# Kernel optimization log

Measured on AMD Instinct MI355X. Metric: run time of the kernel, lower is better.

Reference implementation:

```python
import jax, jax.numpy as jnp
import numpy as np


def make_coord(h, w):
    # LIIF cell-center coordinates in (-1, 1), first axis = rows (height)
    y = -1.0 + (2.0 * jnp.arange(h, dtype=jnp.float32) + 1.0) / h
    x = -1.0 + (2.0 * jnp.arange(w, dtype=jnp.float32) + 1.0) / w
    yy, xx = jnp.meshgrid(y, x, indexing='ij')
    return jnp.stack([yy, xx], axis=-1)  # (h, w, 2)


def gather_nearest(img, coord):
    """Nearest grid_sample, align_corners=False, padding_mode='zeros'.
    img: (b, c, h, w); coord: (b, n, 2) with [...,0]->height, [...,1]->width.
    Returns (b, n, c)."""
    b, c, h, w = img.shape
    iy = jnp.round(((coord[..., 0] + 1.0) * h - 1.0) / 2.0)
    ix = jnp.round(((coord[..., 1] + 1.0) * w - 1.0) / 2.0)
    valid = (iy >= 0) & (iy < h) & (ix >= 0) & (ix < w)
    iyc = jnp.clip(iy, 0, h - 1).astype(jnp.int32)
    ixc = jnp.clip(ix, 0, w - 1).astype(jnp.int32)
    idx = iyc * w + ixc                                  # (b, n)
    flat = img.reshape(b, c, h * w)
    out = jnp.take_along_axis(flat, idx[:, None, :], axis=2)  # (b, c, n)
    out = jnp.transpose(out, (0, 2, 1))                  # (b, n, c)
    return jnp.where(valid[..., None], out, 0.0)


def mlp(x, w1, b1, w2, b2, w3, b3):
    x = jax.nn.relu(x @ w1 + b1)
    x = jax.nn.relu(x @ w2 + b2)
    return x @ w3 + b3


def query_freq(feat, coord, guide, params):
    b, c, h, w = feat.shape
    H, W = guide.shape[2], guide.shape[3]
    feat_coord = make_coord(h, w)                        # (h, w, 2)
    fc_img = jnp.broadcast_to(jnp.transpose(feat_coord, (2, 0, 1))[None], (b, 2, h, w))
    q_guide = gather_nearest(guide, coord)               # (b, N, guide_dim)
    scale = jnp.array([h, w], dtype=feat.dtype)
    preds = []
    for vx in (-1.0, 1.0):
        for vy in (-1.0, 1.0):
            off = jnp.array([vx / h, vy / w], dtype=feat.dtype)
            c_ = coord + off
            q_feat = gather_nearest(feat, c_)            # (b, N, feat_dim)
            q_coord = gather_nearest(fc_img, c_)         # (b, N, 2)
            rel = (coord - q_coord) * scale              # (b, N, 2)
            inp = jnp.concatenate([q_feat, q_guide, rel], axis=-1)
            preds.append(mlp(inp, *params))              # (b, N, NIR_dim)
    preds = jnp.stack(preds, axis=-1)                    # (b, N, NIR_dim, 4)
    weight = jax.nn.softmax(preds[:, :, -1, :], axis=-1) # (b, N, 4)
    ret = jnp.sum(preds[:, :, :-1, :] * weight[:, :, None, :], axis=-1)  # (b, N, NIR_dim-1)
    return jnp.transpose(ret, (0, 2, 1)).reshape(b, -1, H, W)


def setup_inputs() -> dict:
    key = jax.random.key(0)
    ks = jax.random.split(key, 16)
    b, fd, gd = 8, 128, 128
    h = w = 64
    H = W = 128
    feat = jax.random.normal(ks[0], (b, fd, h, w), dtype=jnp.float32)
    hr_guide = jax.random.normal(ks[1], (b, gd, H, W), dtype=jnp.float32)
    coord = jnp.broadcast_to(make_coord(H, W).reshape(1, H * W, 2), (b, H * W, 2))
    in_dim, h1, h2, out_dim = fd + gd + 2, 256, 128, 33

    def lin(k, i, o):
        return jax.random.normal(k, (i, o), dtype=jnp.float32) / np.sqrt(i).astype(np.float32)

    d = {"feat": feat, "coord": coord, "hr_guide": hr_guide,
         "a_w1": lin(ks[2], in_dim, h1), "a_b1": jnp.zeros((h1,), jnp.float32),
         "a_w2": lin(ks[3], h1, h2),     "a_b2": jnp.zeros((h2,), jnp.float32),
         "a_w3": lin(ks[4], h2, out_dim),"a_b3": jnp.zeros((out_dim,), jnp.float32),
         "p_w1": lin(ks[5], in_dim, h1), "p_b1": jnp.zeros((h1,), jnp.float32),
         "p_w2": lin(ks[6], h1, h2),     "p_b2": jnp.zeros((h2,), jnp.float32),
         "p_w3": lin(ks[7], h2, out_dim),"p_b3": jnp.zeros((out_dim,), jnp.float32)}
    return d


def reference(feat, coord, hr_guide, a_w1, a_b1, a_w2, a_b2, a_w3, a_b3,
              p_w1, p_b1, p_w2, p_b2, p_w3, p_b3):
    feat_f = jnp.fft.fftn(feat, axes=(-2, -1))
    guide_f = jnp.fft.fftn(hr_guide, axes=(-2, -1))
    feat_mag, feat_pha = jnp.abs(feat_f), jnp.angle(feat_f)
    guide_mag, guide_pha = jnp.abs(guide_f), jnp.angle(guide_f)
    mag = query_freq(feat_mag, coord, guide_mag, (a_w1, a_b1, a_w2, a_b2, a_w3, a_b3))
    pha = query_freq(feat_pha, coord, guide_pha, (p_w1, p_b1, p_w2, p_b2, p_w3, p_b3))
    ffted = jax.lax.complex(mag * jnp.cos(pha), mag * jnp.sin(pha))
    return jnp.abs(jnp.fft.ifftn(ffted, axes=(-2, -1)))
```

## Files before the change

kernel.cpp:

```cpp
#include <hip/hip_runtime.h>
#include <cmath>

#define TPB 256

static constexpr int   Bn   = 8;
static constexpr int   FD   = 128, GD = 128;
static constexpr int   FH   = 64,  FW = 64;
static constexpr int   GH   = 128, GW = 128;
static constexpr int   NPIX = GH * GW;
static constexpr long  ROWS = (long)Bn * NPIX;
static constexpr int   NH1  = 256, NH2 = 128, NOUT = 33;
static constexpr float TWO_PI = 6.28318530717958647692f;

typedef __attribute__((ext_vector_type(8))) __bf16 bf16x8;
typedef __attribute__((ext_vector_type(4))) float  f32x4;

__global__ __launch_bounds__(TPB)
void k_meta(const float* __restrict__ coord, int* __restrict__ idxb,
            float2* __restrict__ relb) {
    int t = blockIdx.x * TPB + threadIdx.x;
    if (t >= NPIX * 4) return;
    int pix = t >> 2, o = t & 3;
    float cy = coord[pix * 2 + 0], cx = coord[pix * 2 + 1];
    float vx = (o < 2) ? -1.f : 1.f;
    float vy = (o & 1) ? 1.f : -1.f;
    float cyo = cy + vx / 64.f, cxo = cx + vy / 64.f;
    float fy = rintf(((cyo + 1.f) * 64.f - 1.f) * 0.5f);
    float fx = rintf(((cxo + 1.f) * 64.f - 1.f) * 0.5f);
    bool valid = (fy >= 0.f) && (fy < 64.f) && (fx >= 0.f) && (fx < 64.f);
    int iy = min(max((int)fy, 0), 63), ix = min(max((int)fx, 0), 63);
    float qcy = valid ? (-1.f + (2.f * iy + 1.f) / 64.f) : 0.f;
    float qcx = valid ? (-1.f + (2.f * ix + 1.f) / 64.f) : 0.f;
    relb[t] = make_float2((cy - qcy) * 64.f, (cx - qcx) * 64.f);
    idxb[t] = valid ? (iy * 64 + ix) : -1;
}

__global__ __launch_bounds__(TPB)
void k_prep_w1(const float* __restrict__ w1, __bf16* __restrict__ w1t,
               float2* __restrict__ relw) {
    int i = blockIdx.x * TPB + threadIdx.x;
    if (i < 256) relw[i] = make_float2(w1[256 * 256 + i], w1[257 * 256 + i]);
    if (i >= 256 * 256) return;
    int k = i >> 8, n = i & 255;
    float v = w1[k * 256 + n];
    __bf16 h = (__bf16)v;
    __bf16 lo = (__bf16)(v - (float)h);
    int nb = n >> 7, nl = n & 127, st = k >> 5, kb = (k >> 3) & 3, j = k & 7;
    size_t slab = ((size_t)nb * 8 + st) * 8192;
    w1t[slab + 0    + kb * 1024 + nl * 8 + j] = h;
    w1t[slab + 4096 + kb * 1024 + nl * 8 + j] = lo;
}

__global__ __launch_bounds__(TPB)
void k_prep_w2(const float* __restrict__ w2, __bf16* __restrict__ w2t) {
    int i = blockIdx.x * TPB + threadIdx.x;
    if (i >= 256 * 128) return;
    int k = i >> 7, n = i & 127;
    float v = w2[k * 128 + n];
    __bf16 h = (__bf16)v;
    __bf16 lo = (__bf16)(v - (float)h);
    int st = k >> 5, kb = (k >> 3) & 3, j = k & 7;
    size_t slab = (size_t)st * 8192;
    w2t[slab + 0    + kb * 1024 + n * 8 + j] = h;
    w2t[slab + 4096 + kb * 1024 + n * 8 + j] = lo;
}

__global__ __launch_bounds__(TPB)
void k_prep_fftmat(int mode, int P, __bf16* __restrict__ outm) {
    int R, C, ST;
    bool Atype;
    if (mode == 0)      { R = P;   C = 2*P; ST = P >> 5; Atype = false; }
    else if (mode == 1) { R = 2*P; C = 2*P; ST = P >> 4; Atype = true;  }
    else                { R = 256; C = 256; ST = 8;      Atype = (mode == 3); }
    int i = blockIdx.x * TPB + threadIdx.x;
    if (i >= R * C) return;
    int r = i / C, c = i % C;
    float s, co, val;
    if (mode == 0) {
        int pl = (c >= P) ? 1 : 0, v = c - pl * P;
        int kv = (r * v) % P;
        sincosf(TWO_PI * (float)kv / (float)P, &s, &co);
        val = pl ? -s : co;
    } else if (mode == 1) {
        int u = r >> 1, p = r & 1;
        int pl = (c >= P) ? 1 : 0, y = c - pl * P;
        int uy = (u * y) % P;
        sincosf(TWO_PI * (float)uy / (float)P, &s, &co);
        val = (p == 0) ? (pl ? s : co) : (pl ? co : -s);
    } else if (mode == 2) {
        int v = r >> 1, q = r & 1;
        int pl = c >> 7, x = c & 127;
        int vx = (v * x) & 127;
        sincosf(TWO_PI * (float)vx / 128.f, &s, &co);
        val = (q == 0) ? (pl ? s : co) : (pl ? co : -s);
    } else {
        int y = r >> 1, p = r & 1;
        int pl = c >> 7, u = c & 127;
        int uy = (u * y) & 127;
        sincosf(TWO_PI * (float)uy / 128.f, &s, &co);
        val = (p == 0) ? (pl ? -s : co) : (pl ? co : s);
    }
    int blk, lin, kidx;
    if (Atype) { blk = r >> 7; lin = r & 127; kidx = c; }
    else       { blk = c >> 7; lin = c & 127; kidx = r; }
    int st = kidx >> 5, kb = (kidx >> 3) & 3, j = kidx & 7;
    __bf16 h = (__bf16)val;
    __bf16 lo = (__bf16)(val - (float)h);
    size_t base = (((size_t)blk * ST + st) * 2) * 4096 + (size_t)kb * 1024 + lin * 8 + j;
    outm[base] = h;
    outm[base + 4096] = lo;
}

template <int KTOT, int SW, int HROWS>
__global__ __launch_bounds__(TPB)
void k_fft_p1(const float* __restrict__ A, const __bf16* __restrict__ Bc,
              __bf16* __restrict__ Yslab) {
    constexpr int ST     = KTOT / 32;
    constexpr int LOG2H  = (HROWS == 64) ? 6 : 7;
    constexpr int CHUNK  = 64 * SW;
    constexpr int ST2T   = HROWS / 16;
    constexpr int IMGSLB = ST2T * CHUNK;
    __shared__ __align__(16) __bf16 As2[2][4][128][8];
    __shared__ __align__(16) __bf16 Bs2[8192];
    int t = threadIdx.x;
    int bm0 = blockIdx.x * 128;
    int nb  = blockIdx.y;
    int w = t >> 6, l = t & 63;
    int wr = w >> 1, wc = w & 1;
    int lr = l & 15, lk = l >> 4;
    int am = t >> 1, kh = t & 1;
    f32x4 acc[4][4];
    #pragma unroll
    for (int i = 0; i < 4; i++)
        #pragma unroll
        for (int j = 0; j < 4; j++) acc[i][j] = f32x4{0.f, 0.f, 0.f, 0.f};
    for (int st = 0; st < ST; st++) {
        const float* arow = A + (size_t)(bm0 + am) * KTOT + st * 32 + kh * 16;
        float4 va4[4];
        #pragma unroll
        for (int i = 0; i < 4; i++) va4[i] = ((const float4*)arow)[i];
        const float4* wsl = (const float4*)(Bc + ((size_t)nb * ST + st) * 8192);
        float4 bv[4];
        #pragma unroll
        for (int i = 0; i < 4; i++) bv[i] = wsl[i * 256 + t];
        __syncthreads();
        {
            const float* va = (const float*)&va4[0];
            __bf16 h8[16], l8[16];
            #pragma unroll
            for (int j = 0; j < 16; j++) {
                __bf16 h = (__bf16)va[j];
                h8[j] = h;
                l8[j] = (__bf16)(va[j] - (float)h);
            }
            int kb0 = kh * 2;
            *(bf16x8*)&As2[0][kb0][am][0]     = *(bf16x8*)&h8[0];
            *(bf16x8*)&As2[0][kb0 + 1][am][0] = *(bf16x8*)&h8[8];
            *(bf16x8*)&As2[1][kb0][am][0]     = *(bf16x8*)&l8[0];
            *(bf16x8*)&As2[1][kb0 + 1][am][0] = *(bf16x8*)&l8[8];
            float4* bd = (float4*)&Bs2[0];
            #pragma unroll
            for (int i = 0; i < 4; i++) bd[i * 256 + t] = bv[i];
        }
        __syncthreads();
        bf16x8 ah[4], al[4], bh[4], blo[4];
        #pragma unroll
        for (int mf = 0; mf < 4; mf++) {
            int m = wr * 64 + mf * 16 + lr;
            ah[mf] = *(const bf16x8*)&As2[0][lk][m][0];
            al[mf] = *(const bf16x8*)&As2[1][lk][m][0];
        }
        #pragma unroll
        for (int nf = 0; nf < 4; nf++) {
            int n = wc * 64 + nf * 16 + lr;
            bh[nf]  = *(const bf16x8*)&Bs2[(size_t)lk * 1024 + n * 8];
            blo[nf] = *(const bf16x8*)&Bs2[4096 + (size_t)lk * 1024 + n * 8];
        }
        #pragma unroll
        for (int mf = 0; mf < 4; mf++)
            #pragma unroll
            for (int nf = 0; nf < 4; nf++) {
                acc[mf][nf] = __builtin_amdgcn_mfma_f32_16x16x32_bf16(ah[mf], bh[nf],  acc[mf][nf], 0, 0, 0);
                acc[mf][nf] = __builtin_amdgcn_mfma_f32_16x16x32_bf16(ah[mf], blo[nf], acc[mf][nf], 0, 0, 0);
                acc[mf][nf] = __builtin_amdgcn_mfma_f32_16x16x32_bf16(al[mf], bh[nf],  acc[mf][nf], 0, 0, 0);
            }
    }
    #pragma unroll
    for (int nf = 0; nf < 4; nf++) {
        int Cg = nb * 128 + wc * 64 + nf * 16 + lr;
        int plane = Cg / SW;
        int v = Cg % SW;
        #pragma unroll
        for (int mf = 0; mf < 4; mf++)
            #pragma unroll
            for (int r = 0; r < 4; r++) {
                int rloc = wr * 64 + mf * 16 + lk * 4 + r;
                int grow = bm0 + rloc;
                int img = grow >> LOG2H;
                int y = grow & (HROWS - 1);
                int kp = plane * HROWS + y;
                int st2 = kp >> 5, kb2 = (kp >> 3) & 3, j2 = kp & 7;
                size_t a = (size_t)img * IMGSLB + (size_t)st2 * CHUNK
                         + (size_t)kb2 * (SW * 8) + v * 8 + j2;
                float val = acc[mf][nf][r];
                __bf16 h = (__bf16)val;
                Yslab[a] = h;
                Yslab[a + 32 * SW] = (__bf16)(val - (float)h);
            }
    }
}

template <int HROWS, int SW, int EPI>
__global__ __launch_bounds__(TPB)
void k_fft_p2(const __bf16* __restrict__ Ac, const __bf16* __restrict__ Yslab,
              float* __restrict__ out0, float* __restrict__ out1) {
    constexpr int ST2    = HROWS / 16;
    constexpr int CHUNK  = 64 * SW;
    constexpr int IMGSLB = ST2 * CHUNK;
    __shared__ __align__(16) __bf16 As2[2][4][128][8];
    __shared__ __align__(16) __bf16 Bs2[8192];
    int t = threadIdx.x;
    int imgx = blockIdx.x;
    int mb   = blockIdx.y;
    int w = t >> 6, l = t & 63;
    int wr = w >> 1, wc = w & 1;
    int lr = l & 15, lk = l >> 4;
    f32x4 acc[4][4];
    #pragma unroll
    for (int i = 0; i < 4; i++)
        #pragma unroll
        for (int j = 0; j < 4; j++) acc[i][j] = f32x4{0.f, 0.f, 0.f, 0.f};
    for (int st = 0; st < ST2; st++) {
        const float4* asl = (const float4*)(Ac + ((size_t)mb * ST2 + st) * 8192);
        float4 av[4];
        #pragma unroll
        for (int i = 0; i < 4; i++) av[i] = asl[i * 256 + t];
        float4 bv[4];
        if constexpr (EPI == 1) {
            int u_ = t & 127, isel = t >> 7;
            const float4* bsl = (const float4*)(Yslab
                + (size_t)(imgx * 2 + isel) * IMGSLB + (size_t)st * CHUNK);
            #pragma unroll
            for (int i = 0; i < 4; i++) bv[i] = bsl[i * 128 + u_];
        } else {
            const float4* bsl = (const float4*)(Yslab
                + (size_t)imgx * IMGSLB + (size_t)st * CHUNK);
            #pragma unroll
            for (int i = 0; i < 4; i++) bv[i] = bsl[i * 256 + t];
        }
        __syncthreads();
        {
            float4* ad = (float4*)&As2[0][0][0][0];
            #pragma unroll
            for (int i = 0; i < 4; i++) ad[i * 256 + t] = av[i];
            float4* bd = (float4*)&Bs2[0];
            if constexpr (EPI == 1) {
                int u_ = t & 127, isel = t >> 7;
                #pragma unroll
                for (int i = 0; i < 4; i++) {
                    int f = i * 128 + u_;
                    int hlkb = f >> 6, v = f & 63;
                    bd[hlkb * 128 + isel * 64 + v] = bv[i];
                }
            } else {
                #pragma unroll
                for (int i = 0; i < 4; i++) bd[i * 256 + t] = bv[i];
            }
        }
        __syncthreads();
        bf16x8 ah[4], al[4], bh[4], blo[4];
        #pragma unroll
        for (int mf = 0; mf < 4; mf++) {
            int m = wr * 64 + mf * 16 + lr;
            ah[mf] = *(const bf16x8*)&As2[0][lk][m][0];
            al[mf] = *(const bf16x8*)&As2[1][lk][m][0];
        }
        #pragma unroll
        for (int nf = 0; nf < 4; nf++) {
            int n = wc * 64 + nf * 16 + lr;
            bh[nf]  = *(const bf16x8*)&Bs2[(size_t)lk * 1024 + n * 8];
            blo[nf] = *(const bf16x8*)&Bs2[4096 + (size_t)lk * 1024 + n * 8];
        }
        #pragma unroll
        for (int mf = 0; mf < 4; mf++)
            #pragma unroll
            for (int nf = 0; nf < 4; nf++) {
                acc[mf][nf] = __builtin_amdgcn_mfma_f32_16x16x32_bf16(ah[mf], bh[nf],  acc[mf][nf], 0, 0, 0);
                acc[mf][nf] = __builtin_amdgcn_mfma_f32_16x16x32_bf16(ah[mf], blo[nf], acc[mf][nf], 0, 0, 0);
                acc[mf][nf] = __builtin_amdgcn_mfma_f32_16x16x32_bf16(al[mf], bh[nf],  acc[mf][nf], 0, 0, 0);
            }
    }
    #pragma unroll
    for (int nf = 0; nf < 4; nf++) {
        int v = wc * 64 + nf * 16 + lr;
        #pragma unroll
        for (int mf = 0; mf < 4; mf++) {
            int mlocb = wr * 64 + mf * 16 + lk * 4;
            #pragma unroll
            for (int rp = 0; rp < 4; rp += 2) {
                float re = acc[mf][nf][rp], im = acc[mf][nf][rp + 1];
                int m = mb * 128 + mlocb + rp;
                int u = m >> 1;
                if constexpr (EPI == 0) {
                    size_t oi = (size_t)imgx * (HROWS * SW) + (size_t)u * SW + v;
                    out0[oi] = sqrtf(re * re + im * im);
                    out1[oi] = atan2f(im, re);
                } else if constexpr (EPI == 1) {
                    int isel = v >> 6, vv = v & 63;
                    size_t oi = (size_t)(imgx * 2 + isel) * 4096 + (size_t)u * 64 + vv;
                    out0[oi] = sqrtf(re * re + im * im);
                    out1[oi] = atan2f(im, re);
                } else {
                    size_t oi = (size_t)imgx * 16384 + (size_t)u * 128 + v;
                    out0[oi] = sqrtf(re * re + im * im) * (1.f / 16384.f);
                }
            }
        }
    }
}

__global__ __launch_bounds__(TPB)
void k_prep_zc(const float* __restrict__ mag, const float* __restrict__ pha,
               float* __restrict__ Zc) {
    int i = blockIdx.x * TPB + threadIdx.x;
    float m = mag[i], p = pha[i];
    float s, c; sincosf(p, &s, &c);
    Zc[2 * i]     = m * c;
    Zc[2 * i + 1] = m * s;
}

__global__ __launch_bounds__(TPB)
void k_gemm1_mfma(const float* __restrict__ featX, const float* __restrict__ guideX,
                  const int* __restrict__ idxb, const float2* __restrict__ relb,
                  int row0, int ch, const __bf16* __restrict__ w1t,
                  const float2* __restrict__ relw, const float* __restrict__ b1,
                  float* __restrict__ H1c) {
    __shared__ __align__(16) __bf16 As2[2][4][128][8];
    __shared__ __align__(16) __bf16 Bs2[8192];
    __shared__ int    sfo[128];
    __shared__ int    sgo[128];
    __shared__ float2 srel[128];
    int t = threadIdx.x;
    int o = blockIdx.z;
    int bm0 = blockIdx.x * 128;
    int nb  = blockIdx.y;
    int bn0 = nb * 128;
    if (t < 128) {
        int row = row0 + bm0 + t;
        int b = row >> 14, pix = row & 16383;
        int id = idxb[pix * 4 + o];
        sfo[t] = (id >= 0) ? (b * (FD * FH * FW) + id) : -1;
        sgo[t] = b * (GD * GH * GW) + pix;
        srel[t] = relb[pix * 4 + o];
    }
    int w = t >> 6, l = t & 63;
    int wr = w >> 1, wc = w & 1;
    int lr = l & 15, lk = l >> 4;
    int am = t >> 1, kh = t & 1;
    const __bf16* wbase = w1t + (size_t)nb * 65536;
    f32x4 acc[4][4];
    #pragma unroll
    for (int i = 0; i < 4; i++)
        #pragma unroll
        for (int j = 0; j < 4; j++) acc[i][j] = f32x4{0.f, 0.f, 0.f, 0.f};
    __syncthreads();
    for (int st = 0; st < 8; st++) {
        int k0 = st * 32;
        float va[16];
        if (st < 4) {
            int fo = sfo[am];
            int kbase = k0 + kh * 16;
            if (fo >= 0) {
                #pragma unroll
                for (int j = 0; j < 16; j++)
                    va[j] = featX[(size_t)fo + (size_t)(kbase + j) * (FH * FW)];
            } else {
                #pragma unroll
                for (int j = 0; j < 16; j++) va[j] = 0.f;
            }
        } else {
            int go = sgo[am];
            int kbase = k0 - 128 + kh * 16;
            #pragma unroll
            for (int j = 0; j < 16; j++)
                va[j] = guideX[(size_t)go + (size_t)(kbase + j) * (GH * GW)];
        }
        float4 bv[4];
        const float4* wsl = (const float4*)(wbase + (size_t)st * 8192);
        #pragma unroll
        for (int i = 0; i < 4; i++) bv[i] = wsl[i * 256 + t];
        __syncthreads();
        {
            __bf16 h8[16], l8[16];
            #pragma unroll
            for (int j = 0; j < 16; j++) {
                __bf16 h = (__bf16)va[j];
                h8[j] = h;
                l8[j] = (__bf16)(va[j] - (float)h);
            }
            int kb0 = kh * 2;
            *(bf16x8*)&As2[0][kb0][am][0]     = *(bf16x8*)&h8[0];
            *(bf16x8*)&As2[0][kb0 + 1][am][0] = *(bf16x8*)&h8[8];
            *(bf16x8*)&As2[1][kb0][am][0]     = *(bf16x8*)&l8[0];
            *(bf16x8*)&As2[1][kb0 + 1][am][0] = *(bf16x8*)&l8[8];
            float4* bd = (float4*)&Bs2[0];
            #pragma unroll
            for (int i = 0; i < 4; i++) bd[i * 256 + t] = bv[i];
        }
        __syncthreads();
        bf16x8 ah[4], al[4], bh[4], blo[4];
        #pragma unroll
        for (int mf = 0; mf < 4; mf++) {
            int m = wr * 64 + mf * 16 + lr;
            ah[mf] = *(const bf16x8*)&As2[0][lk][m][0];
            al[mf] = *(const bf16x8*)&As2[1][lk][m][0];
        }
        #pragma unroll
        for (int nf = 0; nf < 4; nf++) {
            int n = wc * 64 + nf * 16 + lr;
            bh[nf]  = *(const bf16x8*)&Bs2[(size_t)lk * 1024 + n * 8];
            blo[nf] = *(const bf16x8*)&Bs2[4096 + (size_t)lk * 1024 + n * 8];
        }
        #pragma unroll
        for (int mf = 0; mf < 4; mf++)
            #pragma unroll
            for (int nf = 0; nf < 4; nf++) {
                acc[mf][nf] = __builtin_amdgcn_mfma_f32_16x16x32_bf16(ah[mf], bh[nf],  acc[mf][nf], 0, 0, 0);
                acc[mf][nf] = __builtin_amdgcn_mfma_f32_16x16x32_bf16(ah[mf], blo[nf], acc[mf][nf], 0, 0, 0);
                acc[mf][nf] = __builtin_amdgcn_mfma_f32_16x16x32_bf16(al[mf], bh[nf],  acc[mf][nf], 0, 0, 0);
            }
    }
    #pragma unroll
    for (int nf = 0; nf < 4; nf++) {
        int col = bn0 + wc * 64 + nf * 16 + lr;
        float bias = b1[col];
        float2 rw = relw[col];
        #pragma unroll
        for (int mf = 0; mf < 4; mf++)
            #pragma unroll
            for (int r = 0; r < 4; r++) {
                int rloc = wr * 64 + mf * 16 + lk * 4 + r;
                float2 rr = srel[rloc];
                float v = acc[mf][nf][r] + bias + rr.x * rw.x + rr.y * rw.y;
                H1c[((size_t)o * ch + bm0 + rloc) * NH1 + col] = fmaxf(v, 0.f);
            }
    }
}

__global__ __launch_bounds__(TPB)
void k_gemm2_mfma(const float* __restrict__ A, const __bf16* __restrict__ w2t,
                  const float* __restrict__ b2, float* __restrict__ H2c, int ch) {
    __shared__ __align__(16) __bf16 As2[2][4][128][8];
    __shared__ __align__(16) __bf16 Bs2[8192];
    int t = threadIdx.x;
    int o = blockIdx.z;
    int bm0 = blockIdx.x * 128;
    int w = t >> 6, l = t & 63;
    int wr = w >> 1, wc = w & 1;
    int lr = l & 15, lk = l >> 4;
    int am = t >> 1, kh = t & 1;
    f32x4 acc[4][4];
    #pragma unroll
    for (int i = 0; i < 4; i++)
        #pragma unroll
        for (int j = 0; j < 4; j++) acc[i][j] = f32x4{0.f, 0.f, 0.f, 0.f};
    size_t arow = ((size_t)o * ch + bm0 + am) * NH1;
    for (int st = 0; st < 8; st++) {
        int k0 = st * 32;
        float4 va4[4];
        #pragma unroll
        for (int i = 0; i < 4; i++)
            va4[i] = *(const float4*)&A[arow + k0 + kh * 16 + i * 4];
        float4 bv[4];
        const float4* wsl = (const float4*)(w2t + (size_t)st * 8192);
        #pragma unroll
        for (int i = 0; i < 4; i++) bv[i] = wsl[i * 256 + t];
        __syncthreads();
        {
            const float* va = (const float*)&va4[0];
            __bf16 h8[16], l8[16];
            #pragma unroll
            for (int j = 0; j < 16; j++) {
                __bf16 h = (__bf16)va[j];
                h8[j] = h;
                l8[j] = (__bf16)(va[j] - (float)h);
            }
            int kb0 = kh * 2;
            *(bf16x8*)&As2[0][kb0][am][0]     = *(bf16x8*)&h8[0];
            *(bf16x8*)&As2[0][kb0 + 1][am][0] = *(bf16x8*)&h8[8];
            *(bf16x8*)&As2[1][kb0][am][0]     = *(bf16x8*)&l8[0];
            *(bf16x8*)&As2[1][kb0 + 1][am][0] = *(bf16x8*)&l8[8];
            float4* bd = (float4*)&Bs2[0];
            #pragma unroll
            for (int i = 0; i < 4; i++) bd[i * 256 + t] = bv[i];
        }
        __syncthreads();
        bf16x8 ah[4], al[4], bh[4], blo[4];
        #pragma unroll
        for (int mf = 0; mf < 4; mf++) {
            int m = wr * 64 + mf * 16 + lr;
            ah[mf] = *(const bf16x8*)&As2[0][lk][m][0];
            al[mf] = *(const bf16x8*)&As2[1][lk][m][0];
        }
        #pragma unroll
        for (int nf = 0; nf < 4; nf++) {
            int n = wc * 64 + nf * 16 + lr;
            bh[nf]  = *(const bf16x8*)&Bs2[(size_t)lk * 1024 + n * 8];
            blo[nf] = *(const bf16x8*)&Bs2[4096 + (size_t)lk * 1024 + n * 8];
        }
        #pragma unroll
        for (int mf = 0; mf < 4; mf++)
            #pragma unroll
            for (int nf = 0; nf < 4; nf++) {
                acc[mf][nf] = __builtin_amdgcn_mfma_f32_16x16x32_bf16(ah[mf], bh[nf],  acc[mf][nf], 0, 0, 0);
                acc[mf][nf] = __builtin_amdgcn_mfma_f32_16x16x32_bf16(ah[mf], blo[nf], acc[mf][nf], 0, 0, 0);
                acc[mf][nf] = __builtin_amdgcn_mfma_f32_16x16x32_bf16(al[mf], bh[nf],  acc[mf][nf], 0, 0, 0);
            }
    }
    #pragma unroll
    for (int nf = 0; nf < 4; nf++) {
        int col = wc * 64 + nf * 16 + lr;
        float bias = b2[col];
        #pragma unroll
        for (int mf = 0; mf < 4; mf++)
            #pragma unroll
            for (int r = 0; r < 4; r++) {
                int rloc = wr * 64 + mf * 16 + lk * 4 + r;
                float v = acc[mf][nf][r] + bias;
                H2c[((size_t)o * ch + bm0 + rloc) * NH2 + col] = fmaxf(v, 0.f);
            }
    }
}

template <int BM, int BN, int KTOT, int NACT, bool RELU>
__global__ __launch_bounds__(TPB)
void k_gemm(const float* __restrict__ A, const float* __restrict__ Bw,
            const float* __restrict__ bias, float* __restrict__ C, int chM) {
    constexpr int RT = BM / 16;
    constexpr int CT = BN / 16;
    const float* Az = A + (size_t)blockIdx.z * chM * KTOT;
    float*       Cz = C + (size_t)blockIdx.z * chM * NACT;
    __shared__ float As[8][BM];
    __shared__ float Bs[8][BN];
    int t = threadIdx.x;
    int bm0 = blockIdx.x * BM, bn0 = blockIdx.y * BN;
    int w = t >> 6, l = t & 63;
    int wr = w >> 1, wc = w & 1;
    int tm8 = l >> 3, tn8 = l & 7;
    int fa = wr * (BM / 2) + tm8 * RT;
    int fb = wc * (BN / 2) + tn8 * CT;
    int am, ak;
    if constexpr (BM == 128) { am = t & 127; ak = (t >> 7) * 4; }
    else                     { am = t & 63;  ak = (t >> 6) * 2; }
    constexpr int BNUM = BN / 32;
    int bk = t >> 5, bn = (t & 31) * BNUM;
    float acc[RT][CT] = {};
    for (int k0 = 0; k0 < KTOT; k0 += 8) {
        float avr[4];
        if constexpr (BM == 128) {
            float4 a4 = *reinterpret_cast<const float4*>(
                &Az[(size_t)(bm0 + am) * KTOT + k0 + ak]);
            avr[0] = a4.x; avr[1] = a4.y; avr[2] = a4.z; avr[3] = a4.w;
        } else {
            float2 a2 = *reinterpret_cast<const float2*>(
                &Az[(size_t)(bm0 + am) * KTOT + k0 + ak]);
            avr[0] = a2.x; avr[1] = a2.y;
        }
        float bvr[BNUM];
        #pragma unroll
        for (int j = 0; j < BNUM; j++) {
            int col = bn0 + bn + j;
            bvr[j] = (col < NACT) ? Bw[(size_t)(k0 + bk) * NACT + col] : 0.f;
        }
        __syncthreads();
        if constexpr (BM == 128) {
            As[ak + 0][am] = avr[0]; As[ak + 1][am] = avr[1];
            As[ak + 2][am] = avr[2]; As[ak + 3][am] = avr[3];
        } else {
            As[ak + 0][am] = avr[0]; As[ak + 1][am] = avr[1];
        }
        #pragma unroll
        for (int j = 0; j < BNUM; j++) Bs[bk][bn + j] = bvr[j];
        __syncthreads();
        #pragma unroll
        for (int kk = 0; kk < 8; kk++) {
            float ar[RT], br[CT];
            #pragma unroll
            for (int i = 0; i < RT; i += 4) {
                float4 a4 = *reinterpret_cast<const float4*>(&As[kk][fa + i]);
                ar[i] = a4.x; ar[i + 1] = a4.y; ar[i + 2] = a4.z; ar[i + 3] = a4.w;
            }
            #pragma unroll
            for (int i = 0; i < CT; i += 4) {
                float4 b4 = *reinterpret_cast<const float4*>(&Bs[kk][fb + i]);
                br[i] = b4.x; br[i + 1] = b4.y; br[i + 2] = b4.z; br[i + 3] = b4.w;
            }
            #pragma unroll
            for (int r = 0; r < RT; r++)
                #pragma unroll
                for (int cc = 0; cc < CT; cc++)
                    acc[r][cc] = fmaf(ar[r], br[cc], acc[r][cc]);
        }
    }
    float bb[CT];
    #pragma unroll
    for (int cc = 0; cc < CT; cc++) {
        int col = bn0 + fb + cc;
        bb[cc] = (col < NACT) ? bias[col] : 0.f;
    }
    #pragma unroll
    for (int r = 0; r < RT; r++) {
        size_t row = bm0 + fa + r;
        #pragma unroll
        for (int cc = 0; cc < CT; cc++) {
            int col = bn0 + fb + cc;
            if (col < NACT) {
                float v = acc[r][cc] + bb[cc];
                if (RELU) v = fmaxf(v, 0.f);
                Cz[row * NACT + col] = v;
            }
        }
    }
}

__global__ __launch_bounds__(TPB)
void k_combine(const float* __restrict__ predsC, int row0, int ch,
               float* __restrict__ res) {
    int rl_ = blockIdx.x * TPB + threadIdx.x;
    if (rl_ >= ch) return;
    float p3[4];
    #pragma unroll
    for (int o = 0; o < 4; o++)
        p3[o] = predsC[((size_t)o * ch + rl_) * NOUT + 32];
    float mx = fmaxf(fmaxf(p3[0], p3[1]), fmaxf(p3[2], p3[3]));
    float e[4], sum = 0.f;
    #pragma unroll
    for (int o = 0; o < 4; o++) { e[o] = expf(p3[o] - mx); sum += e[o]; }
    float inv = 1.f / sum;
    int row = row0 + rl_;
    int b = row >> 14, pix = row & 16383;
    float* outb = res + (size_t)b * 32 * NPIX + pix;
    for (int c = 0; c < 32; c++) {
        float acc = 0.f;
        #pragma unroll
        for (int o = 0; o < 4; o++)
            acc = fmaf(predsC[((size_t)o * ch + rl_) * NOUT + c], e[o] * inv, acc);
        outb[(size_t)c * NPIX] = acc;
    }
}

static size_t align256(size_t x) { return (x + 255) & ~(size_t)255; }

static size_t region_bytes(int ch) {
    size_t region = align256((size_t)ch * 4 * NH1 * 4)
                  + align256((size_t)ch * 4 * NH2 * 4)
                  + align256((size_t)ch * 4 * NOUT * 4);
    size_t fftmin = 67108864 + 4096;
    if (region < fftmin) region = fftmin;
    return region;
}

static size_t plan_bytes(int ch) {
    size_t t = align256(region_bytes(ch));
    t += align256((size_t)Bn * FD * FH * FW * 4) * 2;
    t += align256((size_t)Bn * GD * GH * GW * 4) * 2;
    t += align256((size_t)Bn * 32 * NPIX * 4);
    t += align256((size_t)131072 * 2) * 2;
    t += align256((size_t)65536 * 2) * 2;
    t += align256((size_t)256 * 8) * 2;
    t += align256((size_t)NPIX * 4 * 4);
    t += align256((size_t)NPIX * 4 * 8);
    t += align256(32768) + align256(131072);
    t += align256(65536) + align256(262144);
    t += align256(262144) + align256(262144);
    return t;
}

extern "C" void kernel_launch(void* const* d_in, const int* in_sizes, int n_in,
                              void* d_out, int out_size, void* d_ws, size_t ws_size,
                              hipStream_t stream) {
    const float* feat  = (const float*)d_in[0];
    const float* coord = (const float*)d_in[1];
    const float* guide = (const float*)d_in[2];
    const float* aw1 = (const float*)d_in[3];
    const float* ab1 = (const float*)d_in[4];
    const float* aw2 = (const float*)d_in[5];
    const float* ab2 = (const float*)d_in[6];
    const float* aw3 = (const float*)d_in[7];
    const float* ab3 = (const float*)d_in[8];
    const float* pw1 = (const float*)d_in[9];
    const float* pb1 = (const float*)d_in[10];
    const float* pw2 = (const float*)d_in[11];
    const float* pb2 = (const float*)d_in[12];
    const float* pw3 = (const float*)d_in[13];
    const float* pb3 = (const float*)d_in[14];
    float* out = (float*)d_out;

    int ch = 0;
    const int cands[3] = {16384, 8192, 4096};
    for (int i = 0; i < 3; i++)
        if (plan_bytes(cands[i]) <= ws_size) { ch = cands[i]; break; }
    if (ch == 0) return;
    const int nchk = (int)(ROWS / ch);

    char* ws = (char*)d_ws;
    size_t off = 0;
    auto alloc = [&](size_t bytes) -> void* {
        void* p = ws + off;
        off += align256(bytes);
        return p;
    };
    size_t region = region_bytes(ch);
    char*   rbase  = (char*)alloc(region);
    __bf16* Yf     = (__bf16*)rbase;
    __bf16* Yg     = (__bf16*)rbase;
    float*  H1c    = (float*)rbase;
    float*  H2c    = (float*)(rbase + align256((size_t)ch * 4 * NH1 * 4));
    float*  predsC = (float*)(rbase + align256((size_t)ch * 4 * NH1 * 4)
                                    + align256((size_t)ch * 4 * NH2 * 4));
    float*  Zc     = (float*)rbase;
    __bf16* Yi     = (__bf16*)(rbase + 33554432);
    float*  featM  = (float*)alloc((size_t)Bn * FD * FH * FW * 4);
    float*  featP  = (float*)alloc((size_t)Bn * FD * FH * FW * 4);
    float*  guideM = (float*)alloc((size_t)Bn * GD * GH * GW * 4);
    float*  guideP = (float*)alloc((size_t)Bn * GD * GH * GW * 4);
    float*  phares = (float*)alloc((size_t)Bn * 32 * NPIX * 4);
    float*  magres = out;
    __bf16* w1ta   = (__bf16*)alloc((size_t)131072 * 2);
    __bf16* w1tp   = (__bf16*)alloc((size_t)131072 * 2);
    __bf16* w2ta   = (__bf16*)alloc((size_t)65536 * 2);
    __bf16* w2tp   = (__bf16*)alloc((size_t)65536 * 2);
    float2* relwa  = (float2*)alloc((size_t)256 * 8);
    float2* relwp  = (float2*)alloc((size_t)256 * 8);
    int*    idxb   = (int*)alloc((size_t)NPIX * 4 * 4);
    float2* relb   = (float2*)alloc((size_t)NPIX * 4 * 8);
    __bf16* B1f    = (__bf16*)alloc(32768);
    __bf16* B1g    = (__bf16*)alloc(131072);
    __bf16* A2f    = (__bf16*)alloc(65536);
    __bf16* A2g    = (__bf16*)alloc(262144);
    __bf16* iB1    = (__bf16*)alloc(262144);
    __bf16* iA2    = (__bf16*)alloc(262144);

    k_prep_w1<<<(256 * 256 + TPB - 1) / TPB, TPB, 0, stream>>>(aw1, w1ta, relwa);
    k_prep_w1<<<(256 * 256 + TPB - 1) / TPB, TPB, 0, stream>>>(pw1, w1tp, relwp);
    k_prep_w2<<<(256 * 128 + TPB - 1) / TPB, TPB, 0, stream>>>(aw2, w2ta);
    k_prep_w2<<<(256 * 128 + TPB - 1) / TPB, TPB, 0, stream>>>(pw2, w2tp);
    k_meta<<<(NPIX * 4 + TPB - 1) / TPB, TPB, 0, stream>>>(coord, idxb, relb);
    k_prep_fftmat<<<(64 * 128 + TPB - 1) / TPB, TPB, 0, stream>>>(0, 64, B1f);
    k_prep_fftmat<<<(128 * 256 + TPB - 1) / TPB, TPB, 0, stream>>>(0, 128, B1g);
    k_prep_fftmat<<<(128 * 128 + TPB - 1) / TPB, TPB, 0, stream>>>(1, 64, A2f);
    k_prep_fftmat<<<(256 * 256 + TPB - 1) / TPB, TPB, 0, stream>>>(1, 128, A2g);
    k_prep_fftmat<<<(256 * 256 + TPB - 1) / TPB, TPB, 0, stream>>>(2, 128, iB1);
    k_prep_fftmat<<<(256 * 256 + TPB - 1) / TPB, TPB, 0, stream>>>(3, 128, iA2);

    k_fft_p1<64, 64, 64><<<dim3(512, 1), TPB, 0, stream>>>(feat, B1f, Yf);
    k_fft_p2<64, 64, 1><<<dim3(512, 1), TPB, 0, stream>>>(A2f, Yf, featM, featP);
    for (int h = 0; h < 2; h++) {
        size_t ofs = (size_t)h * 512 * NPIX;
        k_fft_p1<128, 128, 128><<<dim3(512, 2), TPB, 0, stream>>>(
            guide + ofs, B1g, Yg);
        k_fft_p2<128, 128, 0><<<dim3(512, 2), TPB, 0, stream>>>(
            A2g, Yg, guideM + ofs, guideP + ofs);
    }

    for (int br = 0; br < 2; br++) {
        const float*  fX   = br ? featP  : featM;
        const float*  gX   = br ? guideP : guideM;
        const __bf16* w1t  = br ? w1tp : w1ta;
        const float2* relw = br ? relwp : relwa;
        const float*  b1   = br ? pb1 : ab1;
        const __bf16* w2t  = br ? w2tp : w2ta;
        const float*  b2   = br ? pb2 : ab2;
        const float*  w3   = br ? pw3 : aw3;
        const float*  b3   = br ? pb3 : ab3;
        float* resb = br ? phares : magres;
        for (int c = 0; c < nchk; c++) {
            int row0 = c * ch;
            k_gemm1_mfma<<<dim3(ch / 128, 2, 4), TPB, 0, stream>>>(
                fX, gX, idxb, relb, row0, ch, w1t, relw, b1, H1c);
            k_gemm2_mfma<<<dim3(ch / 128, 1, 4), TPB, 0, stream>>>(
                H1c, w2t, b2, H2c, ch);
            k_gemm<64, 64, 128, 33, false><<<dim3(ch / 64, 1, 4), TPB, 0, stream>>>(
                H2c, w3, b3, predsC, ch);
            k_combine<<<ch / TPB, TPB, 0, stream>>>(predsC, row0, ch, resb);
        }
    }

    k_prep_zc<<<(256 * NPIX) / TPB, TPB, 0, stream>>>(magres, phares, Zc);
    k_fft_p1<256, 128, 128><<<dim3(256, 2), TPB, 0, stream>>>(Zc, iB1, Yi);
    k_fft_p2<128, 128, 2><<<dim3(256, 2), TPB, 0, stream>>>(iA2, Yi, out, nullptr);
}
```

Before: 3.114 ms.

## Restructure FFT output to channel-last layout and fuse MLP gather, layer 3 and combine

The forward FFTs are rewritten as new k_fft1/k_fft2 kernels that write magnitude and phase in a pixel-major, channel-contiguous layout, so the MLP's first layer can load features with vector reads instead of strided per-channel gathers. The first layer now shares the guide-part GEMM across the four offsets, since the guide term does not depend on the offset. The third layer is moved to MFMA with pre-split bf16 weights and fused with the softmax-weighted combine, which removes the predsC buffer and two kernel launches. The cost is larger transposed intermediate buffers and the extra scatter work in the FFT epilogues.

```diff
diff --git a/kernel.cpp b/kernel.cpp
--- a/kernel.cpp
+++ b/kernel.cpp
@@ -4,8 +4,6 @@
 #define TPB 256
 
 static constexpr int   Bn   = 8;
-static constexpr int   FD   = 128, GD = 128;
-static constexpr int   FH   = 64,  FW = 64;
 static constexpr int   GH   = 128, GW = 128;
 static constexpr int   NPIX = GH * GW;
 static constexpr long  ROWS = (long)Bn * NPIX;
@@ -36,8 +34,8 @@
 }
 
 __global__ __launch_bounds__(TPB)
-void k_prep_w1(const float* __restrict__ w1, __bf16* __restrict__ w1t,
-               float2* __restrict__ relw) {
+void k_prep_w1split(const float* __restrict__ w1, __bf16* __restrict__ w1f,
+                    __bf16* __restrict__ w1g, float2* __restrict__ relw) {
     int i = blockIdx.x * TPB + threadIdx.x;
     if (i < 256) relw[i] = make_float2(w1[256 * 256 + i], w1[257 * 256 + i]);
     if (i >= 256 * 256) return;
@@ -45,10 +43,12 @@
     float v = w1[k * 256 + n];
     __bf16 h = (__bf16)v;
     __bf16 lo = (__bf16)(v - (float)h);
-    int nb = n >> 7, nl = n & 127, st = k >> 5, kb = (k >> 3) & 3, j = k & 7;
-    size_t slab = ((size_t)nb * 8 + st) * 8192;
-    w1t[slab + 0    + kb * 1024 + nl * 8 + j] = h;
-    w1t[slab + 4096 + kb * 1024 + nl * 8 + j] = lo;
+    int part = k >> 7, kl = k & 127;
+    int nb = n >> 7, nl = n & 127, st = kl >> 5, kb = (kl >> 3) & 3, j = kl & 7;
+    __bf16* dst = part ? w1g : w1f;
+    size_t base = (size_t)(nb * 4 + st) * 8192 + kb * 1024 + nl * 8 + j;
+    dst[base] = h;
+    dst[base + 4096] = lo;
 }
 
 __global__ __launch_bounds__(TPB)
@@ -63,6 +63,40 @@
     size_t slab = (size_t)st * 8192;
     w2t[slab + 0    + kb * 1024 + n * 8 + j] = h;
     w2t[slab + 4096 + kb * 1024 + n * 8 + j] = lo;
+}
+
+__global__ __launch_bounds__(TPB)
+void k_prep_w3(const float* __restrict__ w3, __bf16* __restrict__ w3t) {
+    int i = blockIdx.x * TPB + threadIdx.x;
+    if (i >= 128 * 48) return;
+    int k = i / 48, n = i - k * 48;
+    float v = (n < 33) ? w3[k * 33 + n] : 0.f;
+    __bf16 h = (__bf16)v;
+    __bf16 lo = (__bf16)(v - (float)h);
+    int st = k >> 5, kb = (k >> 3) & 3, j = k & 7;
+    size_t base = (size_t)st * 3072 + kb * 384 + n * 8 + j;
+    w3t[base] = h;
+    w3t[base + 1536] = lo;
+}
+
+__global__ __launch_bounds__(TPB)
+void k_prep_fftA1(int P, __bf16* __restrict__ outm) {
+    int i = blockIdx.x * TPB + threadIdx.x;
+    if (i >= 2 * P * P) return;
+    int m = i / P, x = i - m * P;
+    int pl = (m >= P) ? 1 : 0;
+    int vv = m - pl * P;
+    int xv = (x * vv) % P;
+    float s, c; sincosf(TWO_PI * (float)xv / (float)P, &s, &c);
+    float val = pl ? -s : c;
+    __bf16 h = (__bf16)val;
+    __bf16 lo = (__bf16)(val - (float)h);
+    int mb = m >> 7, ml = m & 127;
+    int ST = P >> 5;
+    int st = x >> 5, kb = (x >> 3) & 3, j = x & 7;
+    size_t base = (size_t)(mb * ST + st) * 8192 + kb * 1024 + ml * 8 + j;
+    outm[base] = h;
+    outm[base + 4096] = lo;
 }
 
 __global__ __launch_bounds__(TPB)
@@ -111,6 +145,185 @@
     outm[base + 4096] = lo;
 }
 
+template <int P>
+__global__ __launch_bounds__(TPB)
+void k_fft1(const float* __restrict__ in, const __bf16* __restrict__ A1,
+            float* __restrict__ Z1, int b0) {
+    constexpr int LOG2P = (P == 64) ? 6 : 7;
+    constexpr int ST = P / 32;
+    __shared__ __align__(16) __bf16 As2[8192];
+    __shared__ __align__(16) __bf16 Bs2[8192];
+    int t = threadIdx.x;
+    int bid = blockIdx.x;
+    int brel = bid >> LOG2P, y = bid & (P - 1);
+    int b = b0 + brel;
+    int mb = blockIdx.y;
+    int w = t >> 6, l = t & 63;
+    int wr = w >> 1, wc = w & 1;
+    int lr = l & 15, lk = l >> 4;
+    int cs = t >> 1, kh = t & 1;
+    f32x4 acc[4][4];
+    #pragma unroll
+    for (int i = 0; i < 4; i++)
+        #pragma unroll
+        for (int j = 0; j < 4; j++) acc[i][j] = f32x4{0.f, 0.f, 0.f, 0.f};
+    for (int st = 0; st < ST; st++) {
+        const float4* dp = (const float4*)&in[((size_t)(b * 128 + cs) * P + y) * P
+                                             + st * 32 + kh * 16];
+        float4 va4[4];
+        #pragma unroll
+        for (int i = 0; i < 4; i++) va4[i] = dp[i];
+        const float4* asl = (const float4*)(A1 + (size_t)(mb * ST + st) * 8192);
+        float4 av[4];
+        #pragma unroll
+        for (int i = 0; i < 4; i++) av[i] = asl[i * 256 + t];
+        __syncthreads();
+        {
+            const float* va = (const float*)&va4[0];
+            __bf16 h8[16], l8[16];
+            #pragma unroll
+            for (int j = 0; j < 16; j++) {
+                __bf16 h = (__bf16)va[j];
+                h8[j] = h;
+                l8[j] = (__bf16)(va[j] - (float)h);
+            }
+            int kb0 = kh * 2;
+            *(bf16x8*)&Bs2[(kb0    ) * 1024 + cs * 8] = *(bf16x8*)&h8[0];
+            *(bf16x8*)&Bs2[(kb0 + 1) * 1024 + cs * 8] = *(bf16x8*)&h8[8];
+            *(bf16x8*)&Bs2[4096 + (kb0    ) * 1024 + cs * 8] = *(bf16x8*)&l8[0];
+            *(bf16x8*)&Bs2[4096 + (kb0 + 1) * 1024 + cs * 8] = *(bf16x8*)&l8[8];
+            float4* ad = (float4*)&As2[0];
+            #pragma unroll
+            for (int i = 0; i < 4; i++) ad[i * 256 + t] = av[i];
+        }
+        __syncthreads();
+        bf16x8 ah[4], al[4], bh[4], blo[4];
+        #pragma unroll
+        for (int mf = 0; mf < 4; mf++) {
+            int m = wr * 64 + mf * 16 + lr;
+            ah[mf] = *(const bf16x8*)&As2[lk * 1024 + m * 8];
+            al[mf] = *(const bf16x8*)&As2[4096 + lk * 1024 + m * 8];
+        }
+        #pragma unroll
+        for (int nf = 0; nf < 4; nf++) {
+            int n = wc * 64 + nf * 16 + lr;
+            bh[nf]  = *(const bf16x8*)&Bs2[lk * 1024 + n * 8];
+            blo[nf] = *(const bf16x8*)&Bs2[4096 + lk * 1024 + n * 8];
+        }
+        #pragma unroll
+        for (int mf = 0; mf < 4; mf++)
+            #pragma unroll
+            for (int nf = 0; nf < 4; nf++) {
+                acc[mf][nf] = __builtin_amdgcn_mfma_f32_16x16x32_bf16(ah[mf], bh[nf],  acc[mf][nf], 0, 0, 0);
+                acc[mf][nf] = __builtin_amdgcn_mfma_f32_16x16x32_bf16(ah[mf], blo[nf], acc[mf][nf], 0, 0, 0);
+                acc[mf][nf] = __builtin_amdgcn_mfma_f32_16x16x32_bf16(al[mf], bh[nf],  acc[mf][nf], 0, 0, 0);
+            }
+    }
+    #pragma unroll
+    for (int nf = 0; nf < 4; nf++) {
+        int c = wc * 64 + nf * 16 + lr;
+        #pragma unroll
+        for (int mf = 0; mf < 4; mf++)
+            #pragma unroll
+            for (int r = 0; r < 4; r++) {
+                int m = mb * 128 + wr * 64 + mf * 16 + lk * 4 + r;
+                int pl = m >> LOG2P, v = m & (P - 1);
+                int kp = pl * P + y;
+                Z1[(((size_t)brel * P + v) * (2 * P) + kp) * 128 + c] = acc[mf][nf][r];
+            }
+    }
+}
+
+template <int P>
+__global__ __launch_bounds__(TPB)
+void k_fft2(const __bf16* __restrict__ A2, const float* __restrict__ Z1,
+            float* __restrict__ outM, float* __restrict__ outP, int b0) {
+    constexpr int LOG2P = (P == 64) ? 6 : 7;
+    constexpr int ST2 = P / 16;
+    __shared__ __align__(16) __bf16 As2[8192];
+    __shared__ __align__(16) __bf16 Bs2[8192];
+    int t = threadIdx.x;
+    int bid = blockIdx.x;
+    int brel = bid >> LOG2P, v = bid & (P - 1);
+    int b = b0 + brel;
+    int mb = blockIdx.y;
+    int w = t >> 6, l = t & 63;
+    int wr = w >> 1, wc = w & 1;
+    int lr = l & 15, lk = l >> 4;
+    int kq = t >> 3, cq = (t & 7) * 16;
+    f32x4 acc[4][4];
+    #pragma unroll
+    for (int i = 0; i < 4; i++)
+        #pragma unroll
+        for (int j = 0; j < 4; j++) acc[i][j] = f32x4{0.f, 0.f, 0.f, 0.f};
+    size_t zbase = ((size_t)brel * P + v) * (2 * P) * 128;
+    for (int st = 0; st < ST2; st++) {
+        const float4* zp = (const float4*)&Z1[zbase + (size_t)(st * 32 + kq) * 128 + cq];
+        float4 z4[4];
+        #pragma unroll
+        for (int i = 0; i < 4; i++) z4[i] = zp[i];
+        const float4* asl = (const float4*)(A2 + (size_t)(mb * ST2 + st) * 8192);
+        float4 av[4];
+        #pragma unroll
+        for (int i = 0; i < 4; i++) av[i] = asl[i * 256 + t];
+        __syncthreads();
+        {
+            const float* zz = (const float*)&z4[0];
+            int kb = kq >> 3, j = kq & 7;
+            #pragma unroll
+            for (int i = 0; i < 16; i++) {
+                float val = zz[i];
+                __bf16 h = (__bf16)val;
+                __bf16 lo = (__bf16)(val - (float)h);
+                int c = cq + i;
+                Bs2[kb * 1024 + c * 8 + j] = h;
+                Bs2[4096 + kb * 1024 + c * 8 + j] = lo;
+            }
+            float4* ad = (float4*)&As2[0];
+            #pragma unroll
+            for (int i = 0; i < 4; i++) ad[i * 256 + t] = av[i];
+        }
+        __syncthreads();
+        bf16x8 ah[4], al[4], bh[4], blo[4];
+        #pragma unroll
+        for (int mf = 0; mf < 4; mf++) {
+            int m = wr * 64 + mf * 16 + lr;
+            ah[mf] = *(const bf16x8*)&As2[lk * 1024 + m * 8];
+            al[mf] = *(const bf16x8*)&As2[4096 + lk * 1024 + m * 8];
+        }
+        #pragma unroll
+        for (int nf = 0; nf < 4; nf++) {
+            int n = wc * 64 + nf * 16 + lr;
+            bh[nf]  = *(const bf16x8*)&Bs2[lk * 1024 + n * 8];
+            blo[nf] = *(const bf16x8*)&Bs2[4096 + lk * 1024 + n * 8];
+        }
+        #pragma unroll
+        for (int mf = 0; mf < 4; mf++)
+            #pragma unroll
+            for (int nf = 0; nf < 4; nf++) {
+                acc[mf][nf] = __builtin_amdgcn_mfma_f32_16x16x32_bf16(ah[mf], bh[nf],  acc[mf][nf], 0, 0, 0);
+                acc[mf][nf] = __builtin_amdgcn_mfma_f32_16x16x32_bf16(ah[mf], blo[nf], acc[mf][nf], 0, 0, 0);
+                acc[mf][nf] = __builtin_amdgcn_mfma_f32_16x16x32_bf16(al[mf], bh[nf],  acc[mf][nf], 0, 0, 0);
+            }
+    }
+    #pragma unroll
+    for (int nf = 0; nf < 4; nf++) {
+        int c = wc * 64 + nf * 16 + lr;
+        #pragma unroll
+        for (int mf = 0; mf < 4; mf++) {
+            int mlocb = mb * 128 + wr * 64 + mf * 16 + lk * 4;
+            #pragma unroll
+            for (int rp = 0; rp < 4; rp += 2) {
+                float re = acc[mf][nf][rp], im = acc[mf][nf][rp + 1];
+                int u = (mlocb + rp) >> 1;
+                size_t oi = ((size_t)b * (P * P) + u * P + v) * 128 + c;
+                outM[oi] = sqrtf(re * re + im * im);
+                outP[oi] = atan2f(im, re);
+            }
+        }
+    }
+}
+
 template <int KTOT, int SW, int HROWS>
 __global__ __launch_bounds__(TPB)
 void k_fft_p1(const float* __restrict__ A, const __bf16* __restrict__ Bc,
@@ -235,37 +448,19 @@
         float4 av[4];
         #pragma unroll
         for (int i = 0; i < 4; i++) av[i] = asl[i * 256 + t];
+        const float4* bsl = (const float4*)(Yslab
+            + (size_t)imgx * IMGSLB + (size_t)st * CHUNK);
         float4 bv[4];
-        if constexpr (EPI == 1) {
-            int u_ = t & 127, isel = t >> 7;
-            const float4* bsl = (const float4*)(Yslab
-                + (size_t)(imgx * 2 + isel) * IMGSLB + (size_t)st * CHUNK);
-            #pragma unroll
-            for (int i = 0; i < 4; i++) bv[i] = bsl[i * 128 + u_];
-        } else {
-            const float4* bsl = (const float4*)(Yslab
-                + (size_t)imgx * IMGSLB + (size_t)st * CHUNK);
-            #pragma unroll
-            for (int i = 0; i < 4; i++) bv[i] = bsl[i * 256 + t];
-        }
+        #pragma unroll
+        for (int i = 0; i < 4; i++) bv[i] = bsl[i * 256 + t];
         __syncthreads();
         {
             float4* ad = (float4*)&As2[0][0][0][0];
             #pragma unroll
             for (int i = 0; i < 4; i++) ad[i * 256 + t] = av[i];
             float4* bd = (float4*)&Bs2[0];
-            if constexpr (EPI == 1) {
-                int u_ = t & 127, isel = t >> 7;
-                #pragma unroll
-                for (int i = 0; i < 4; i++) {
-                    int f = i * 128 + u_;
-                    int hlkb = f >> 6, v = f & 63;
-                    bd[hlkb * 128 + isel * 64 + v] = bv[i];
-                }
-            } else {
-                #pragma unroll
-                for (int i = 0; i < 4; i++) bd[i * 256 + t] = bv[i];
-            }
+            #pragma unroll
+            for (int i = 0; i < 4; i++) bd[i * 256 + t] = bv[i];
         }
         __syncthreads();
         bf16x8 ah[4], al[4], bh[4], blo[4];
@@ -301,19 +496,8 @@
                 float re = acc[mf][nf][rp], im = acc[mf][nf][rp + 1];
                 int m = mb * 128 + mlocb + rp;
                 int u = m >> 1;
-                if constexpr (EPI == 0) {
-                    size_t oi = (size_t)imgx * (HROWS * SW) + (size_t)u * SW + v;
-                    out0[oi] = sqrtf(re * re + im * im);
-                    out1[oi] = atan2f(im, re);
-                } else if constexpr (EPI == 1) {
-                    int isel = v >> 6, vv = v & 63;
-                    size_t oi = (size_t)(imgx * 2 + isel) * 4096 + (size_t)u * 64 + vv;
-                    out0[oi] = sqrtf(re * re + im * im);
-                    out1[oi] = atan2f(im, re);
-                } else {
-                    size_t oi = (size_t)imgx * 16384 + (size_t)u * 128 + v;
-                    out0[oi] = sqrtf(re * re + im * im) * (1.f / 16384.f);
-                }
+                size_t oi = (size_t)imgx * 16384 + (size_t)u * 128 + v;
+                out0[oi] = sqrtf(re * re + im * im) * (1.f / 16384.f);
             }
         }
     }
@@ -330,99 +514,84 @@
 }
 
 __global__ __launch_bounds__(TPB)
-void k_gemm1_mfma(const float* __restrict__ featX, const float* __restrict__ guideX,
-                  const int* __restrict__ idxb, const float2* __restrict__ relb,
-                  int row0, int ch, const __bf16* __restrict__ w1t,
-                  const float2* __restrict__ relw, const float* __restrict__ b1,
-                  float* __restrict__ H1c) {
-    __shared__ __align__(16) __bf16 As2[2][4][128][8];
+void k_gemm1f(const float* __restrict__ featT, const float* __restrict__ guideT,
+              const int* __restrict__ idxb, const float2* __restrict__ relb,
+              int row0, int ch,
+              const __bf16* __restrict__ w1f, const __bf16* __restrict__ w1g,
+              const float2* __restrict__ relw, const float* __restrict__ b1,
+              float* __restrict__ H1c) {
+    __shared__ __align__(16) __bf16 As2[4096];
     __shared__ __align__(16) __bf16 Bs2[8192];
-    __shared__ int    sfo[128];
-    __shared__ int    sgo[128];
-    __shared__ float2 srel[128];
+    __shared__ int    sfo[4][64];
+    __shared__ float2 srel[4][64];
     int t = threadIdx.x;
-    int o = blockIdx.z;
-    int bm0 = blockIdx.x * 128;
+    int bm0 = blockIdx.x * 64;
     int nb  = blockIdx.y;
-    int bn0 = nb * 128;
-    if (t < 128) {
-        int row = row0 + bm0 + t;
-        int b = row >> 14, pix = row & 16383;
+    {
+        int o = t >> 6, r = t & 63;
+        int grow = row0 + bm0 + r;
+        int b = grow >> 14, pix = grow & 16383;
         int id = idxb[pix * 4 + o];
-        sfo[t] = (id >= 0) ? (b * (FD * FH * FW) + id) : -1;
-        sgo[t] = b * (GD * GH * GW) + pix;
-        srel[t] = relb[pix * 4 + o];
+        sfo[o][r] = (id >= 0) ? (b * 4096 + id) : -1;
+        srel[o][r] = relb[pix * 4 + o];
     }
     int w = t >> 6, l = t & 63;
     int wr = w >> 1, wc = w & 1;
     int lr = l & 15, lk = l >> 4;
-    int am = t >> 1, kh = t & 1;
-    const __bf16* wbase = w1t + (size_t)nb * 65536;
-    f32x4 acc[4][4];
-    #pragma unroll
-    for (int i = 0; i < 4; i++)
+    int rs = t & 63, kq = t >> 6;
+    float bb[4]; float2 rw[4];
+    #pragma unroll
+    for (int nf = 0; nf < 4; nf++) {
+        int col = nb * 128 + wc * 64 + nf * 16 + lr;
+        bb[nf] = b1[col];
+        rw[nf] = relw[col];
+    }
+    f32x4 acc[2][4], gb[2][4];
+    #pragma unroll
+    for (int i = 0; i < 2; i++)
         #pragma unroll
         for (int j = 0; j < 4; j++) acc[i][j] = f32x4{0.f, 0.f, 0.f, 0.f};
     __syncthreads();
-    for (int st = 0; st < 8; st++) {
-        int k0 = st * 32;
-        float va[16];
-        if (st < 4) {
-            int fo = sfo[am];
-            int kbase = k0 + kh * 16;
-            if (fo >= 0) {
-                #pragma unroll
-                for (int j = 0; j < 16; j++)
-                    va[j] = featX[(size_t)fo + (size_t)(kbase + j) * (FH * FW)];
-            } else {
-                #pragma unroll
-                for (int j = 0; j < 16; j++) va[j] = 0.f;
-            }
-        } else {
-            int go = sgo[am];
-            int kbase = k0 - 128 + kh * 16;
-            #pragma unroll
-            for (int j = 0; j < 16; j++)
-                va[j] = guideX[(size_t)go + (size_t)(kbase + j) * (GH * GW)];
-        }
+    size_t arowg = (size_t)(row0 + bm0 + rs) * 128;
+    for (int st = 0; st < 4; st++) {
+        const float4* ap = (const float4*)&guideT[arowg + st * 32 + kq * 8];
+        float4 a0 = ap[0], a1 = ap[1];
+        const float4* wsl = (const float4*)(w1g + (size_t)(nb * 4 + st) * 8192);
         float4 bv[4];
-        const float4* wsl = (const float4*)(wbase + (size_t)st * 8192);
         #pragma unroll
         for (int i = 0; i < 4; i++) bv[i] = wsl[i * 256 + t];
         __syncthreads();
         {
-            __bf16 h8[16], l8[16];
-            #pragma unroll
-            for (int j = 0; j < 16; j++) {
+            float va[8] = {a0.x, a0.y, a0.z, a0.w, a1.x, a1.y, a1.z, a1.w};
+            __bf16 h8[8], l8[8];
+            #pragma unroll
+            for (int j = 0; j < 8; j++) {
                 __bf16 h = (__bf16)va[j];
                 h8[j] = h;
                 l8[j] = (__bf16)(va[j] - (float)h);
             }
-            int kb0 = kh * 2;
-            *(bf16x8*)&As2[0][kb0][am][0]     = *(bf16x8*)&h8[0];
-            *(bf16x8*)&As2[0][kb0 + 1][am][0] = *(bf16x8*)&h8[8];
-            *(bf16x8*)&As2[1][kb0][am][0]     = *(bf16x8*)&l8[0];
-            *(bf16x8*)&As2[1][kb0 + 1][am][0] = *(bf16x8*)&l8[8];
+            *(bf16x8*)&As2[kq * 512 + rs * 8] = *(bf16x8*)&h8[0];
+            *(bf16x8*)&As2[2048 + kq * 512 + rs * 8] = *(bf16x8*)&l8[0];
             float4* bd = (float4*)&Bs2[0];
             #pragma unroll
             for (int i = 0; i < 4; i++) bd[i * 256 + t] = bv[i];
         }
         __syncthreads();
-        bf16x8 ah[4], al[4], bh[4], blo[4];
-        #pragma unroll
-        for (int mf = 0; mf < 4; mf++) {
-            int m = wr * 64 + mf * 16 + lr;
-            ah[mf] = *(const bf16x8*)&As2[0][lk][m][0];
-            al[mf] = *(const bf16x8*)&As2[1][lk][m][0];
+        bf16x8 ah[2], al[2], bh[4], blo[4];
+        #pragma unroll
+        for (int mf = 0; mf < 2; mf++) {
+            int m = wr * 32 + mf * 16 + lr;
+            ah[mf] = *(const bf16x8*)&As2[lk * 512 + m * 8];
+            al[mf] = *(const bf16x8*)&As2[2048 + lk * 512 + m * 8];
         }
         #pragma unroll
         for (int nf = 0; nf < 4; nf++) {
             int n = wc * 64 + nf * 16 + lr;
-            bh[nf]  = *(const bf16x8*)&Bs2[(size_t)lk * 1024 + n * 8];
-            blo[nf] = *(const bf16x8*)&Bs2[4096 + (size_t)lk * 1024 + n * 8];
-        }
-        #pragma unroll
-        for (int mf = 0; mf < 4; mf++)
+            bh[nf]  = *(const bf16x8*)&Bs2[lk * 1024 + n * 8];
+            blo[nf] = *(const bf16x8*)&Bs2[4096 + lk * 1024 + n * 8];
+        }
+        #pragma unroll
+        for (int mf = 0; mf < 2; mf++)
             #pragma unroll
             for (int nf = 0; nf < 4; nf++) {
                 acc[mf][nf] = __builtin_amdgcn_mfma_f32_16x16x32_bf16(ah[mf], bh[nf],  acc[mf][nf], 0, 0, 0);
@@ -431,19 +600,79 @@
             }
     }
     #pragma unroll
-    for (int nf = 0; nf < 4; nf++) {
-        int col = bn0 + wc * 64 + nf * 16 + lr;
-        float bias = b1[col];
-        float2 rw = relw[col];
-        #pragma unroll
-        for (int mf = 0; mf < 4; mf++)
-            #pragma unroll
-            for (int r = 0; r < 4; r++) {
-                int rloc = wr * 64 + mf * 16 + lk * 4 + r;
-                float2 rr = srel[rloc];
-                float v = acc[mf][nf][r] + bias + rr.x * rw.x + rr.y * rw.y;
-                H1c[((size_t)o * ch + bm0 + rloc) * NH1 + col] = fmaxf(v, 0.f);
-            }
+    for (int i = 0; i < 2; i++)
+        #pragma unroll
+        for (int j = 0; j < 4; j++) gb[i][j] = acc[i][j];
+    for (int o = 0; o < 4; o++) {
+        #pragma unroll
+        for (int i = 0; i < 2; i++)
+            #pragma unroll
+            for (int j = 0; j < 4; j++) acc[i][j] = gb[i][j];
+        int fo = sfo[o][rs];
+        for (int st = 0; st < 4; st++) {
+            float4 a0, a1;
+            if (fo >= 0) {
+                const float4* ap = (const float4*)&featT[(size_t)fo * 128 + st * 32 + kq * 8];
+                a0 = ap[0]; a1 = ap[1];
+            } else {
+                a0 = make_float4(0.f, 0.f, 0.f, 0.f); a1 = a0;
+            }
+            const float4* wsl = (const float4*)(w1f + (size_t)(nb * 4 + st) * 8192);
+            float4 bv[4];
+            #pragma unroll
+            for (int i = 0; i < 4; i++) bv[i] = wsl[i * 256 + t];
+            __syncthreads();
+            {
+                float va[8] = {a0.x, a0.y, a0.z, a0.w, a1.x, a1.y, a1.z, a1.w};
+                __bf16 h8[8], l8[8];
+                #pragma unroll
+                for (int j = 0; j < 8; j++) {
+                    __bf16 h = (__bf16)va[j];
+                    h8[j] = h;
+                    l8[j] = (__bf16)(va[j] - (float)h);
+                }
+                *(bf16x8*)&As2[kq * 512 + rs * 8] = *(bf16x8*)&h8[0];
+                *(bf16x8*)&As2[2048 + kq * 512 + rs * 8] = *(bf16x8*)&l8[0];
+                float4* bd = (float4*)&Bs2[0];
+                #pragma unroll
+                for (int i = 0; i < 4; i++) bd[i * 256 + t] = bv[i];
+            }
+            __syncthreads();
+            bf16x8 ah[2], al[2], bh[4], blo[4];
+            #pragma unroll
+            for (int mf = 0; mf < 2; mf++) {
+                int m = wr * 32 + mf * 16 + lr;
+                ah[mf] = *(const bf16x8*)&As2[lk * 512 + m * 8];
+                al[mf] = *(const bf16x8*)&As2[2048 + lk * 512 + m * 8];
+            }
+            #pragma unroll
+            for (int nf = 0; nf < 4; nf++) {
+                int n = wc * 64 + nf * 16 + lr;
+                bh[nf]  = *(const bf16x8*)&Bs2[lk * 1024 + n * 8];
+                blo[nf] = *(const bf16x8*)&Bs2[4096 + lk * 1024 + n * 8];
+            }
+            #pragma unroll
+            for (int mf = 0; mf < 2; mf++)
+                #pragma unroll
+                for (int nf = 0; nf < 4; nf++) {
+                    acc[mf][nf] = __builtin_amdgcn_mfma_f32_16x16x32_bf16(ah[mf], bh[nf],  acc[mf][nf], 0, 0, 0);
+                    acc[mf][nf] = __builtin_amdgcn_mfma_f32_16x16x32_bf16(ah[mf], blo[nf], acc[mf][nf], 0, 0, 0);
+                    acc[mf][nf] = __builtin_amdgcn_mfma_f32_16x16x32_bf16(al[mf], bh[nf],  acc[mf][nf], 0, 0, 0);
+                }
+        }
+        #pragma unroll
+        for (int nf = 0; nf < 4; nf++) {
+            int col = nb * 128 + wc * 64 + nf * 16 + lr;
+            #pragma unroll
+            for (int mf = 0; mf < 2; mf++)
+                #pragma unroll
+                for (int r = 0; r < 4; r++) {
+                    int rloc = wr * 32 + mf * 16 + lk * 4 + r;
+                    float2 rr = srel[o][rloc];
+                    float v = acc[mf][nf][r] + bb[nf] + rr.x * rw[nf].x + rr.y * rw[nf].y;
+                    H1c[((size_t)o * ch + bm0 + rloc) * NH1 + col] = fmaxf(v, 0.f);
+                }
+        }
     }
 }
 
@@ -532,120 +761,107 @@
     }
 }
 
-template <int BM, int BN, int KTOT, int NACT, bool RELU>
-__global__ __launch_bounds__(TPB)
-void k_gemm(const float* __restrict__ A, const float* __restrict__ Bw,
-            const float* __restrict__ bias, float* __restrict__ C, int chM) {
-    constexpr int RT = BM / 16;
-    constexpr int CT = BN / 16;
-    const float* Az = A + (size_t)blockIdx.z * chM * KTOT;
-    float*       Cz = C + (size_t)blockIdx.z * chM * NACT;
-    __shared__ float As[8][BM];
-    __shared__ float Bs[8][BN];
+__global__ __launch_bounds__(TPB)
+void k_g3c(const float* __restrict__ H2c, const __bf16* __restrict__ w3t,
+           const float* __restrict__ b3, int row0, int ch,
+           float* __restrict__ res) {
+    __shared__ __align__(16) __bf16 As2[4096];
+    __shared__ __align__(16) __bf16 Bs3[3072];
+    __shared__ float p3s[4][64];
     int t = threadIdx.x;
-    int bm0 = blockIdx.x * BM, bn0 = blockIdx.y * BN;
+    int bm0 = blockIdx.x * 64;
     int w = t >> 6, l = t & 63;
-    int wr = w >> 1, wc = w & 1;
-    int tm8 = l >> 3, tn8 = l & 7;
-    int fa = wr * (BM / 2) + tm8 * RT;
-    int fb = wc * (BN / 2) + tn8 * CT;
-    int am, ak;
-    if constexpr (BM == 128) { am = t & 127; ak = (t >> 7) * 4; }
-    else                     { am = t & 63;  ak = (t >> 6) * 2; }
-    constexpr int BNUM = BN / 32;
-    int bk = t >> 5, bn = (t & 31) * BNUM;
-    float acc[RT][CT] = {};
-    for (int k0 = 0; k0 < KTOT; k0 += 8) {
-        float avr[4];
-        if constexpr (BM == 128) {
-            float4 a4 = *reinterpret_cast<const float4*>(
-                &Az[(size_t)(bm0 + am) * KTOT + k0 + ak]);
-            avr[0] = a4.x; avr[1] = a4.y; avr[2] = a4.z; avr[3] = a4.w;
-        } else {
-            float2 a2 = *reinterpret_cast<const float2*>(
-                &Az[(size_t)(bm0 + am) * KTOT + k0 + ak]);
-            avr[0] = a2.x; avr[1] = a2.y;
-        }
-        float bvr[BNUM];
-        #pragma unroll
-        for (int j = 0; j < BNUM; j++) {
-            int col = bn0 + bn + j;
-            bvr[j] = (col < NACT) ? Bw[(size_t)(k0 + bk) * NACT + col] : 0.f;
-        }
-        __syncthreads();
-        if constexpr (BM == 128) {
-            As[ak + 0][am] = avr[0]; As[ak + 1][am] = avr[1];
-            As[ak + 2][am] = avr[2]; As[ak + 3][am] = avr[3];
-        } else {
-            As[ak + 0][am] = avr[0]; As[ak + 1][am] = avr[1];
-        }
-        #pragma unroll
-        for (int j = 0; j < BNUM; j++) Bs[bk][bn + j] = bvr[j];
-        __syncthreads();
-        #pragma unroll
-        for (int kk = 0; kk < 8; kk++) {
-            float ar[RT], br[CT];
-            #pragma unroll
-            for (int i = 0; i < RT; i += 4) {
-                float4 a4 = *reinterpret_cast<const float4*>(&As[kk][fa + i]);
-                ar[i] = a4.x; ar[i + 1] = a4.y; ar[i + 2] = a4.z; ar[i + 3] = a4.w;
-            }
-            #pragma unroll
-            for (int i = 0; i < CT; i += 4) {
-                float4 b4 = *reinterpret_cast<const float4*>(&Bs[kk][fb + i]);
-                br[i] = b4.x; br[i + 1] = b4.y; br[i + 2] = b4.z; br[i + 3] = b4.w;
-            }
-            #pragma unroll
-            for (int r = 0; r < RT; r++)
+    int lr = l & 15, lk = l >> 4;
+    int rs = t & 63, kq = t >> 6;
+    f32x4 acc[4][3];
+    #pragma unroll
+    for (int o = 0; o < 4; o++)
+        #pragma unroll
+        for (int j = 0; j < 3; j++) acc[o][j] = f32x4{0.f, 0.f, 0.f, 0.f};
+    #pragma unroll
+    for (int o = 0; o < 4; o++) {
+        for (int st = 0; st < 4; st++) {
+            const float4* ap = (const float4*)&H2c[((size_t)o * ch + bm0 + rs) * NH2
+                                                   + st * 32 + kq * 8];
+            float4 a0 = ap[0], a1 = ap[1];
+            const float4* wsl = (const float4*)(w3t + (size_t)st * 3072);
+            float4 bv0 = wsl[t];
+            float4 bv1;
+            if (t < 128) bv1 = wsl[256 + t];
+            __syncthreads();
+            {
+                float va[8] = {a0.x, a0.y, a0.z, a0.w, a1.x, a1.y, a1.z, a1.w};
+                __bf16 h8[8], l8[8];
                 #pragma unroll
-                for (int cc = 0; cc < CT; cc++)
-                    acc[r][cc] = fmaf(ar[r], br[cc], acc[r][cc]);
-        }
-    }
-    float bb[CT];
-    #pragma unroll
-    for (int cc = 0; cc < CT; cc++) {
-        int col = bn0 + fb + cc;
-        bb[cc] = (col < NACT) ? bias[col] : 0.f;
-    }
-    #pragma unroll
-    for (int r = 0; r < RT; r++) {
-        size_t row = bm0 + fa + r;
-        #pragma unroll
-        for (int cc = 0; cc < CT; cc++) {
-            int col = bn0 + fb + cc;
-            if (col < NACT) {
-                float v = acc[r][cc] + bb[cc];
-                if (RELU) v = fmaxf(v, 0.f);
-                Cz[row * NACT + col] = v;
-            }
-        }
-    }
-}
-
-__global__ __launch_bounds__(TPB)
-void k_combine(const float* __restrict__ predsC, int row0, int ch,
-               float* __restrict__ res) {
-    int rl_ = blockIdx.x * TPB + threadIdx.x;
-    if (rl_ >= ch) return;
-    float p3[4];
-    #pragma unroll
-    for (int o = 0; o < 4; o++)
-        p3[o] = predsC[((size_t)o * ch + rl_) * NOUT + 32];
-    float mx = fmaxf(fmaxf(p3[0], p3[1]), fmaxf(p3[2], p3[3]));
-    float e[4], sum = 0.f;
-    #pragma unroll
-    for (int o = 0; o < 4; o++) { e[o] = expf(p3[o] - mx); sum += e[o]; }
-    float inv = 1.f / sum;
-    int row = row0 + rl_;
-    int b = row >> 14, pix = row & 16383;
-    float* outb = res + (size_t)b * 32 * NPIX + pix;
-    for (int c = 0; c < 32; c++) {
-        float acc = 0.f;
+                for (int j = 0; j < 8; j++) {
+                    __bf16 h = (__bf16)va[j];
+                    h8[j] = h;
+                    l8[j] = (__bf16)(va[j] - (float)h);
+                }
+                *(bf16x8*)&As2[kq * 512 + rs * 8] = *(bf16x8*)&h8[0];
+                *(bf16x8*)&As2[2048 + kq * 512 + rs * 8] = *(bf16x8*)&l8[0];
+                ((float4*)Bs3)[t] = bv0;
+                if (t < 128) ((float4*)Bs3)[256 + t] = bv1;
+            }
+            __syncthreads();
+            bf16x8 ah, al, bh[3], blo[3];
+            {
+                int m = w * 16 + lr;
+                ah = *(const bf16x8*)&As2[lk * 512 + m * 8];
+                al = *(const bf16x8*)&As2[2048 + lk * 512 + m * 8];
+            }
+            #pragma unroll
+            for (int nf = 0; nf < 3; nf++) {
+                int n = nf * 16 + lr;
+                bh[nf]  = *(const bf16x8*)&Bs3[lk * 384 + n * 8];
+                blo[nf] = *(const bf16x8*)&Bs3[1536 + lk * 384 + n * 8];
+            }
+            #pragma unroll
+            for (int nf = 0; nf < 3; nf++) {
+                acc[o][nf] = __builtin_amdgcn_mfma_f32_16x16x32_bf16(ah, bh[nf],  acc[o][nf], 0, 0, 0);
+                acc[o][nf] = __builtin_amdgcn_mfma_f32_16x16x32_bf16(ah, blo[nf], acc[o][nf], 0, 0, 0);
+                acc[o][nf] = __builtin_amdgcn_mfma_f32_16x16x32_bf16(al, bh[nf],  acc[o][nf], 0, 0, 0);
+            }
+        }
+    }
+    float b32 = b3[32];
+    if (lr == 0) {
         #pragma unroll
         for (int o = 0; o < 4; o++)
-            acc = fmaf(predsC[((size_t)o * ch + rl_) * NOUT + c], e[o] * inv, acc);
-        outb[(size_t)c * NPIX] = acc;
+            #pragma unroll
+            for (int r = 0; r < 4; r++)
+                p3s[o][w * 16 + lk * 4 + r] = acc[o][2][r] + b32;
+    }
+    __syncthreads();
+    float wgt[4][4];
+    #pragma unroll
+    for (int r = 0; r < 4; r++) {
+        int row = w * 16 + lk * 4 + r;
+        float p0 = p3s[0][row], p1 = p3s[1][row], p2 = p3s[2][row], p3v = p3s[3][row];
+        float mx = fmaxf(fmaxf(p0, p1), fmaxf(p2, p3v));
+        float e0 = expf(p0 - mx), e1 = expf(p1 - mx);
+        float e2 = expf(p2 - mx), e3 = expf(p3v - mx);
+        float inv = 1.f / (e0 + e1 + e2 + e3);
+        wgt[r][0] = e0 * inv; wgt[r][1] = e1 * inv;
+        wgt[r][2] = e2 * inv; wgt[r][3] = e3 * inv;
+    }
+    int grow0 = row0 + bm0 + w * 16 + lk * 4;
+    int b = grow0 >> 14, pix0 = grow0 & 16383;
+    #pragma unroll
+    for (int nf = 0; nf < 2; nf++) {
+        int col = nf * 16 + lr;
+        float bc = b3[col];
+        float4 o4;
+        float* po = (float*)&o4;
+        #pragma unroll
+        for (int r = 0; r < 4; r++) {
+            float val = 0.f;
+            #pragma unroll
+            for (int o = 0; o < 4; o++)
+                val = fmaf(acc[o][nf][r] + bc, wgt[r][o], val);
+            po[r] = val;
+        }
+        *(float4*)&res[((size_t)b * 32 + col) * 16384 + pix0] = o4;
     }
 }
 
@@ -653,8 +869,7 @@
 
 static size_t region_bytes(int ch) {
     size_t region = align256((size_t)ch * 4 * NH1 * 4)
-                  + align256((size_t)ch * 4 * NH2 * 4)
-                  + align256((size_t)ch * 4 * NOUT * 4);
+                  + align256((size_t)ch * 4 * NH2 * 4);
     size_t fftmin = 67108864 + 4096;
     if (region < fftmin) region = fftmin;
     return region;
@@ -662,12 +877,13 @@
 
 static size_t plan_bytes(int ch) {
     size_t t = align256(region_bytes(ch));
-    t += align256((size_t)Bn * FD * FH * FW * 4) * 2;
-    t += align256((size_t)Bn * GD * GH * GW * 4) * 2;
+    t += align256((size_t)Bn * 4096 * 128 * 4) * 2;
+    t += align256((size_t)Bn * NPIX * 128 * 4) * 2;
     t += align256((size_t)Bn * 32 * NPIX * 4);
-    t += align256((size_t)131072 * 2) * 2;
-    t += align256((size_t)65536 * 2) * 2;
-    t += align256((size_t)256 * 8) * 2;
+    t += align256(131072) * 4;
+    t += align256(262144) * 2;
+    t += align256(24576) * 2;
+    t += align256(2048) * 2;
     t += align256((size_t)NPIX * 4 * 4);
     t += align256((size_t)NPIX * 4 * 8);
     t += align256(32768) + align256(131072);
@@ -711,78 +927,79 @@
         return p;
     };
     size_t region = region_bytes(ch);
-    char*   rbase  = (char*)alloc(region);
-    __bf16* Yf     = (__bf16*)rbase;
-    __bf16* Yg     = (__bf16*)rbase;
-    float*  H1c    = (float*)rbase;
-    float*  H2c    = (float*)(rbase + align256((size_t)ch * 4 * NH1 * 4));
-    float*  predsC = (float*)(rbase + align256((size_t)ch * 4 * NH1 * 4)
-                                    + align256((size_t)ch * 4 * NH2 * 4));
-    float*  Zc     = (float*)rbase;
-    __bf16* Yi     = (__bf16*)(rbase + 33554432);
-    float*  featM  = (float*)alloc((size_t)Bn * FD * FH * FW * 4);
-    float*  featP  = (float*)alloc((size_t)Bn * FD * FH * FW * 4);
-    float*  guideM = (float*)alloc((size_t)Bn * GD * GH * GW * 4);
-    float*  guideP = (float*)alloc((size_t)Bn * GD * GH * GW * 4);
-    float*  phares = (float*)alloc((size_t)Bn * 32 * NPIX * 4);
-    float*  magres = out;
-    __bf16* w1ta   = (__bf16*)alloc((size_t)131072 * 2);
-    __bf16* w1tp   = (__bf16*)alloc((size_t)131072 * 2);
-    __bf16* w2ta   = (__bf16*)alloc((size_t)65536 * 2);
-    __bf16* w2tp   = (__bf16*)alloc((size_t)65536 * 2);
-    float2* relwa  = (float2*)alloc((size_t)256 * 8);
-    float2* relwp  = (float2*)alloc((size_t)256 * 8);
-    int*    idxb   = (int*)alloc((size_t)NPIX * 4 * 4);
-    float2* relb   = (float2*)alloc((size_t)NPIX * 4 * 8);
-    __bf16* B1f    = (__bf16*)alloc(32768);
-    __bf16* B1g    = (__bf16*)alloc(131072);
-    __bf16* A2f    = (__bf16*)alloc(65536);
-    __bf16* A2g    = (__bf16*)alloc(262144);
-    __bf16* iB1    = (__bf16*)alloc(262144);
-    __bf16* iA2    = (__bf16*)alloc(262144);
-
-    k_prep_w1<<<(256 * 256 + TPB - 1) / TPB, TPB, 0, stream>>>(aw1, w1ta, relwa);
-    k_prep_w1<<<(256 * 256 + TPB - 1) / TPB, TPB, 0, stream>>>(pw1, w1tp, relwp);
+    char*   rbase   = (char*)alloc(region);
+    float*  Z1      = (float*)rbase;
+    float*  H1c     = (float*)rbase;
+    float*  H2c     = (float*)(rbase + align256((size_t)ch * 4 * NH1 * 4));
+    float*  Zc      = (float*)rbase;
+    __bf16* Yi      = (__bf16*)(rbase + 33554432);
+    float*  featTM  = (float*)alloc((size_t)Bn * 4096 * 128 * 4);
+    float*  featTP  = (float*)alloc((size_t)Bn * 4096 * 128 * 4);
+    float*  guideTM = (float*)alloc((size_t)Bn * NPIX * 128 * 4);
+    float*  guideTP = (float*)alloc((size_t)Bn * NPIX * 128 * 4);
+    float*  phares  = (float*)alloc((size_t)Bn * 32 * NPIX * 4);
+    float*  magres  = out;
+    __bf16* w1fa    = (__bf16*)alloc(131072);
+    __bf16* w1ga    = (__bf16*)alloc(131072);
+    __bf16* w1fp    = (__bf16*)alloc(131072);
+    __bf16* w1gp    = (__bf16*)alloc(131072);
+    __bf16* w2ta    = (__bf16*)alloc(262144);
+    __bf16* w2tp    = (__bf16*)alloc(262144);
+    __bf16* w3ta    = (__bf16*)alloc(24576);
+    __bf16* w3tp    = (__bf16*)alloc(24576);
+    float2* relwa   = (float2*)alloc(2048);
+    float2* relwp   = (float2*)alloc(2048);
+    int*    idxb    = (int*)alloc((size_t)NPIX * 4 * 4);
+    float2* relb    = (float2*)alloc((size_t)NPIX * 4 * 8);
+    __bf16* A1f     = (__bf16*)alloc(32768);
+    __bf16* A1g     = (__bf16*)alloc(131072);
+    __bf16* A2f     = (__bf16*)alloc(65536);
+    __bf16* A2g     = (__bf16*)alloc(262144);
+    __bf16* iB1     = (__bf16*)alloc(262144);
+    __bf16* iA2     = (__bf16*)alloc(262144);
+
+    k_prep_w1split<<<(256 * 256 + TPB - 1) / TPB, TPB, 0, stream>>>(aw1, w1fa, w1ga, relwa);
+    k_prep_w1split<<<(256 * 256 + TPB - 1) / TPB, TPB, 0, stream>>>(pw1, w1fp, w1gp, relwp);
     k_prep_w2<<<(256 * 128 + TPB - 1) / TPB, TPB, 0, stream>>>(aw2, w2ta);
     k_prep_w2<<<(256 * 128 + TPB - 1) / TPB, TPB, 0, stream>>>(pw2, w2tp);
+    k_prep_w3<<<(128 * 48 + TPB - 1) / TPB, TPB, 0, stream>>>(aw3, w3ta);
+    k_prep_w3<<<(128 * 48 + TPB - 1) / TPB, TPB, 0, stream>>>(pw3, w3tp);
     k_meta<<<(NPIX * 4 + TPB - 1) / TPB, TPB, 0, stream>>>(coord, idxb, relb);
-    k_prep_fftmat<<<(64 * 128 + TPB - 1) / TPB, TPB, 0, stream>>>(0, 64, B1f);
-    k_prep_fftmat<<<(128 * 256 + TPB - 1) / TPB, TPB, 0, stream>>>(0, 128, B1g);
+    k_prep_fftA1<<<(2 * 64 * 64 + TPB - 1) / TPB, TPB, 0, stream>>>(64, A1f);
+    k_prep_fftA1<<<(2 * 128 * 128 + TPB - 1) / TPB, TPB, 0, stream>>>(128, A1g);
     k_prep_fftmat<<<(128 * 128 + TPB - 1) / TPB, TPB, 0, stream>>>(1, 64, A2f);
     k_prep_fftmat<<<(256 * 256 + TPB - 1) / TPB, TPB, 0, stream>>>(1, 128, A2g);
     k_prep_fftmat<<<(256 * 256 + TPB - 1) / TPB, TPB, 0, stream>>>(2, 128, iB1);
     k_prep_fftmat<<<(256 * 256 + TPB - 1) / TPB, TPB, 0, stream>>>(3, 128, iA2);
 
-    k_fft_p1<64, 64, 64><<<dim3(512, 1), TPB, 0, stream>>>(feat, B1f, Yf);
-    k_fft_p2<64, 64, 1><<<dim3(512, 1), TPB, 0, stream>>>(A2f, Yf, featM, featP);
-    for (int h = 0; h < 2; h++) {
-        size_t ofs = (size_t)h * 512 * NPIX;
-        k_fft_p1<128, 128, 128><<<dim3(512, 2), TPB, 0, stream>>>(
-            guide + ofs, B1g, Yg);
-        k_fft_p2<128, 128, 0><<<dim3(512, 2), TPB, 0, stream>>>(
-            A2g, Yg, guideM + ofs, guideP + ofs);
+    k_fft1<64><<<dim3(512, 1), TPB, 0, stream>>>(feat, A1f, Z1, 0);
+    k_fft2<64><<<dim3(512, 1), TPB, 0, stream>>>(A2f, Z1, featTM, featTP, 0);
+    for (int bp = 0; bp < 4; bp++) {
+        int b0 = bp * 2;
+        k_fft1<128><<<dim3(256, 2), TPB, 0, stream>>>(guide, A1g, Z1, b0);
+        k_fft2<128><<<dim3(256, 2), TPB, 0, stream>>>(A2g, Z1, guideTM, guideTP, b0);
     }
 
     for (int br = 0; br < 2; br++) {
-        const float*  fX   = br ? featP  : featM;
-        const float*  gX   = br ? guideP : guideM;
-        const __bf16* w1t  = br ? w1tp : w1ta;
+        const float*  fT   = br ? featTP  : featTM;
+        const float*  gT   = br ? guideTP : guideTM;
+        const __bf16* w1f  = br ? w1fp : w1fa;
+        const __bf16* w1g  = br ? w1gp : w1ga;
         const float2* relw = br ? relwp : relwa;
         const float*  b1   = br ? pb1 : ab1;
         const __bf16* w2t  = br ? w2tp : w2ta;
         const float*  b2   = br ? pb2 : ab2;
-        const float*  w3   = br ? pw3 : aw3;
+        const __bf16* w3t  = br ? w3tp : w3ta;
         const float*  b3   = br ? pb3 : ab3;
         float* resb = br ? phares : magres;
         for (int c = 0; c < nchk; c++) {
             int row0 = c * ch;
-            k_gemm1_mfma<<<dim3(ch / 128, 2, 4), TPB, 0, stream>>>(
-                fX, gX, idxb, relb, row0, ch, w1t, relw, b1, H1c);
+            k_gemm1f<<<dim3(ch / 64, 2), TPB, 0, stream>>>(
+                fT, gT, idxb, relb, row0, ch, w1f, w1g, relw, b1, H1c);
             k_gemm2_mfma<<<dim3(ch / 128, 1, 4), TPB, 0, stream>>>(
                 H1c, w2t, b2, H2c, ch);
-            k_gemm<64, 64, 128, 33, false><<<dim3(ch / 64, 1, 4), TPB, 0, stream>>>(
-                H2c, w3, b3, predsC, ch);
-            k_combine<<<ch / TPB, TPB, 0, stream>>>(predsC, row0, ch, resb);
+            k_g3c<<<dim3(ch / 64), TPB, 0, stream>>>(
+                H2c, w3t, b3, row0, ch, resb);
         }
     }
 
```

Result: faster. 2.998 ms (-3.7%).
